# Kernel optimization log

Measured on AMD Instinct MI355X. Metric: run time of the kernel, lower is better.

Reference implementation:

```python
import jax, jax.numpy as jnp
import numpy as np

L, B, C = 512, 64, 512  # seq_len, batch, tags_size


def setup_inputs() -> dict:
    key = jax.random.key(0)
    k1, k2, k3, k4, k5, k6 = jax.random.split(key, 6)
    std = (1.0 / C) ** 0.5
    emit = jax.random.normal(k1, (L, B, C), dtype=jnp.float32)
    trans = jax.random.normal(k2, (C, C), dtype=jnp.float32) * std
    trans_from_start = jax.random.normal(k3, (C,), dtype=jnp.float32) * std
    trans_to_end = jax.random.normal(k4, (C,), dtype=jnp.float32) * std
    target = jax.random.randint(k5, (L, B), 0, C)
    # left-aligned length mask so mask.sum(0)-1 indexes the last valid step
    lens = jax.random.randint(k6, (B,), L // 2, L + 1)
    mask = jnp.arange(L)[:, None] < lens[None, :]
    return {"emit": emit, "target": target, "mask": mask, "trans": trans,
            "trans_from_start": trans_from_start, "trans_to_end": trans_to_end}


def _log_z(emit, mask, trans, trans_from_start, trans_to_end):
    log_alpha0 = emit[0] + trans_from_start  # (B, C)

    def step(log_alpha, xs):
        e_i, m_i = xs  # (B, C), (B,)
        # scores[b, j] = logsumexp_i( log_alpha[b, i] + trans[i, j] + e_i[b, j] )
        s = jax.nn.logsumexp(log_alpha[:, :, None] + trans[None, :, :] + e_i[:, None, :], axis=1)
        log_alpha = jnp.where(m_i[:, None], s, log_alpha)
        return log_alpha, None

    log_alpha, _ = jax.lax.scan(step, log_alpha0, (emit[1:], mask[1:]))
    return jax.nn.logsumexp(log_alpha + trans_to_end, axis=1).sum()


def _score(emit, target, mask, trans, trans_from_start, trans_to_end):
    l, b, c = emit.shape
    tr = trans[target[:-1], target[1:]]  # (L-1, B)
    scores = jnp.concatenate([jnp.zeros((1, b), emit.dtype), tr], axis=0)
    scores = scores + jnp.take_along_axis(emit, target[:, :, None], axis=2)[..., 0]
    score = jnp.where(mask, scores, jnp.zeros((), emit.dtype)).sum()
    ends = mask.sum(axis=0) - 1  # (B,) index of last valid step
    last_tags = target[ends, jnp.arange(b)]
    score = score + trans_from_start[target[0]].sum() + trans_to_end[last_tags].sum()
    return score


def reference(emit, target, mask, trans, trans_from_start, trans_to_end):
    b = emit.shape[1]
    log_z = _log_z(emit, mask, trans, trans_from_start, trans_to_end)
    score = _score(emit, target, mask, trans, trans_from_start, trans_to_end)
    return (log_z - score) / b
```

## Files before the change

kernel.cpp:

```cpp
#include <hip/hip_runtime.h>
#include <hip/hip_bf16.h>
#include <stdint.h>

#define LL 512
#define BB 64
#define CC 512
#define TM 255

typedef float float4v __attribute__((ext_vector_type(4)));
typedef int   int4v   __attribute__((ext_vector_type(4)));
typedef unsigned int uint4v __attribute__((ext_vector_type(4)));
typedef int   int8v  __attribute__((ext_vector_type(8)));

#define WS_ET     262144
#define WS_SCORE  524288
#define WS_SVA    524292
#define WS_SVB    524548
#define WS_ALPHA  528384
#define WS_BETA   659456


__device__ __forceinline__ bool mask_at(const void* maskp, bool is_byte, int t, int b) {
    if (is_byte) return ((const unsigned char*)maskp)[t * BB + b] != 0;
    return ((const int*)maskp)[t * BB + b] != 0;
}

__device__ __forceinline__ float rowmax16_dpp(float x) {
    int t;
    t = __builtin_amdgcn_update_dpp(0, __float_as_int(x), 0x128, 0xF, 0xF, true);
    x = fmaxf(x, __int_as_float(t));
    t = __builtin_amdgcn_update_dpp(0, __float_as_int(x), 0x124, 0xF, 0xF, true);
    x = fmaxf(x, __int_as_float(t));
    t = __builtin_amdgcn_update_dpp(0, __float_as_int(x), 0x122, 0xF, 0xF, true);
    x = fmaxf(x, __int_as_float(t));
    t = __builtin_amdgcn_update_dpp(0, __float_as_int(x), 0x121, 0xF, 0xF, true);
    x = fmaxf(x, __int_as_float(t));
    return x;
}

__device__ __forceinline__ void step_barrier() {
    asm volatile("s_waitcnt lgkmcnt(0)" ::: "memory");
    __builtin_amdgcn_sched_barrier(0);
    __builtin_amdgcn_s_barrier();
    asm volatile("" ::: "memory");
}

__global__ void prep_kernel(const float* __restrict__ trans, unsigned char* __restrict__ ws) {
    int g = blockIdx.x * blockDim.x + threadIdx.x;
    if (g == 0) *(float*)(ws + WS_SCORE) = 0.0f;
    if (g >= 512 * 128) return;
    int n  = g & 511;
    int pd = g >> 9;
    int wv = pd >> 4, rw = pd & 15;
    float f[4], ft[4];
#pragma unroll
    for (int nt = 0; nt < 4; ++nt) {
        int k = 64 * wv + 16 * nt + rw;
        f[nt]  = __expf(trans[(size_t)k * CC + n]);
        ft[nt] = __expf(trans[(size_t)n * CC + k]);
    }
    int r = 0;
    r = __builtin_amdgcn_cvt_pk_fp8_f32(f[0], f[1], r, false);
    r = __builtin_amdgcn_cvt_pk_fp8_f32(f[2], f[3], r, true);
    ((int*)ws)[n * 128 + pd] = r;
    int r2 = 0;
    r2 = __builtin_amdgcn_cvt_pk_fp8_f32(ft[0], ft[1], r2, false);
    r2 = __builtin_amdgcn_cvt_pk_fp8_f32(ft[2], ft[3], r2, true);
    ((int*)(ws + WS_ET))[n * 128 + pd] = r2;
}

__launch_bounds__(512, 2)
__global__ void crf_scan_kernel(const float* __restrict__ emit,
                                const int* __restrict__ target,
                                const void* __restrict__ maskp,
                                const float* __restrict__ trans,
                                const float* __restrict__ tfs,
                                const float* __restrict__ t2e,
                                unsigned char* __restrict__ ws) {
    const int tid = threadIdx.x;
    const bool is_byte = ((const unsigned char*)maskp)[1] != 0;

    if (blockIdx.x >= 8) {
        int sb = blockIdx.x - 8;
        float val = 0.0f;
        for (int e = sb * 512 + tid; e < LL * BB; e += 32 * 512) {
            int t = e >> 6, b = e & 63;
            if (mask_at(maskp, is_byte, t, b)) {
                int tg  = target[t * BB + b];
                float v = emit[(size_t)(t * BB + b) * CC + tg];
                if (t > 0) v += trans[(size_t)target[(t - 1) * BB + b] * CC + tg];
                val += v;
            }
        }
        if (sb == 0 && tid < BB) {
            int b = tid;
            val += tfs[target[b]];
            int lo = 0, hi = LL;
            while (lo < hi) {
                int mid = (lo + hi) >> 1;
                if (mask_at(maskp, is_byte, mid, b)) lo = mid + 1; else hi = mid;
            }
            val += t2e[target[(lo - 1) * BB + b]];
        }
        for (int off = 32; off > 0; off >>= 1) val += __shfl_down(val, off);
        if ((tid & 63) == 0) atomicAdd((float*)(ws + WS_SCORE), val);
        return;
    }

    const bool is_fwd = blockIdx.x < 4;
    const int B0 = (is_fwd ? blockIdx.x : blockIdx.x - 4) * 16;

    __shared__ __align__(16) unsigned char p8[2][16 * 528];
    __shared__ __align__(16) float mslotW[2][8][16];
    __shared__ float m0S[16];
    __shared__ float red[16][32];
    __shared__ int   lenS[16];
    __shared__ float mInitS;

    const int wv   = tid >> 6;
    const int lane = tid & 63;
    const int q    = lane >> 4;
    const int r15  = lane & 15;

    const unsigned char* ews = ws + (is_fwd ? 0 : WS_ET);
    int8v ef[4][4];
#pragma unroll
    for (int nt = 0; nt < 4; ++nt) {
        int n = (wv * 4 + nt) * 16 + r15;
#pragma unroll
        for (int kk4 = 0; kk4 < 4; ++kk4) {
            const unsigned char* src = ews + n * 512 + kk4 * 128 + q * 32;
            int4v lo = *(const int4v*)(src);
            int4v hi = *(const int4v*)(src + 16);
            ef[nt][kk4] = __builtin_shufflevector(lo, hi, 0, 1, 2, 3, 4, 5, 6, 7);
        }
    }

    const int c5 = tid >> 5;
    const int s5 = tid & 31;

    if (is_fwd) {
        {
            float lmax = -3.0e38f;
#pragma unroll
            for (int i = 0; i < 4; ++i) {
                int j4 = s5 + 32 * i;
                float4v em = *(const float4v*)(emit + (size_t)(B0 + c5) * CC + 4 * j4);
                float4v tf = *(const float4v*)(tfs + 4 * j4);
                float4v a = em + tf;
                lmax = fmaxf(lmax, fmaxf(fmaxf(a.x, a.y), fmaxf(a.z, a.w)));
            }
            red[c5][s5] = lmax;
        }
        __syncthreads();
        if (tid < 16) {
            float m0 = red[tid][0];
            for (int s = 1; s < 32; ++s) m0 = fmaxf(m0, red[tid][s]);
            m0S[tid] = m0;
        }
        if (tid < 128) ((float*)&mslotW[0][0][0])[tid] = 1.0f;
        __syncthreads();
        {
            float m0 = m0S[c5];
#pragma unroll
            for (int i = 0; i < 4; ++i) {
                int pd = s5 + 32 * i;
                int wvv = pd >> 4, rw = pd & 15;
                float f[4];
#pragma unroll
                for (int nt = 0; nt < 4; ++nt) {
                    int k = 64 * wvv + 16 * nt + rw;
                    f[nt] = __expf(emit[(size_t)(B0 + c5) * CC + k] + tfs[k] - m0);
                }
                int r = 0;
                r = __builtin_amdgcn_cvt_pk_fp8_f32(f[0], f[1], r, false);
                r = __builtin_amdgcn_cvt_pk_fp8_f32(f[2], f[3], r, true);
                *(int*)(&p8[0][0] + c5 * 528 + pd * 4) = r;
            }
        }
        __syncthreads();
    } else {
        {
            float m = t2e[tid];
            for (int off = 32; off > 0; off >>= 1) m = fmaxf(m, __shfl_xor(m, off));
            if (lane == 0) ((float*)red)[wv] = m;
        }
        __syncthreads();
        if (tid == 0) {
            float m = ((float*)red)[0];
            for (int i = 1; i < 8; ++i) m = fmaxf(m, ((float*)red)[i]);
            mInitS = __expf(m);
        }
        __syncthreads();
        {
#pragma unroll
            for (int i = 0; i < 4; ++i) {
                int pd = s5 + 32 * i;
                int wvv = pd >> 4, rw = pd & 15;
                float f[4];
#pragma unroll
                for (int nt = 0; nt < 4; ++nt)
                    f[nt] = __expf(t2e[64 * wvv + 16 * nt + rw]);
                int r = 0;
                r = __builtin_amdgcn_cvt_pk_fp8_f32(f[0], f[1], r, false);
                r = __builtin_amdgcn_cvt_pk_fp8_f32(f[2], f[3], r, true);
                *(int*)(&p8[0][0] + c5 * 528 + pd * 4) = r;
                *(int*)(&p8[1][0] + c5 * 528 + pd * 4) = r;
            }
            int part = 0;
            for (int k = 0; k < 16; ++k)
                part += mask_at(maskp, is_byte, s5 * 16 + k, B0 + c5) ? 1 : 0;
            red[c5][s5] = (float)part;
        }
        __syncthreads();
        if (tid < 16) {
            int s = 0;
            for (int i = 0; i < 32; ++i) s += (int)red[tid][i];
            lenS[tid] = s;
        }
        __syncthreads();
    }

    int4v gsum = {0, 0, 0, 0};
    const float4v z4 = {0.f, 0.f, 0.f, 0.f};

    if (is_fwd) {
        const float* eb0 = emit + (size_t)(BB + B0 + q * 4) * CC + (wv * 64 + r15);
        const float* eb1 = eb0 + 2 * CC;
        float4v ex4[4];
#pragma unroll
        for (int nt = 0; nt < 4; ++nt) {
            ex4[nt][0] = __expf(eb0[0 * CC + nt * 16]);
            ex4[nt][1] = __expf(eb0[1 * CC + nt * 16]);
            ex4[nt][2] = __expf(eb1[0 * CC + nt * 16]);
            ex4[nt][3] = __expf(eb1[1 * CC + nt * 16]);
        }

#pragma unroll 2
        for (int t = 1; t <= TM; ++t) {
            const int wp = t & 1;
            const int rp = wp ^ 1;
            eb0 += BB * CC;
            eb1 += BB * CC;

            const unsigned char* pr = &p8[rp][0] + r15 * 528 + q * 32;
            int8v af[4];
#pragma unroll
            for (int kk4 = 0; kk4 < 4; ++kk4) {
                int4v lo = *(const int4v*)(pr + kk4 * 128);
                int4v hi = *(const int4v*)(pr + kk4 * 128 + 16);
                af[kk4] = __builtin_shufflevector(lo, hi, 0, 1, 2, 3, 4, 5, 6, 7);
            }

            const char* mb = (const char*)&mslotW[(t - 1) & 1][0][q * 4];
            uint4v mm = *(const uint4v*)(mb);
#pragma unroll
            for (int i = 1; i < 8; ++i)
                mm = __builtin_elementwise_max(mm, *(const uint4v*)(mb + i * 64));

            float4v emn4[4];
#pragma unroll
            for (int nt = 0; nt < 4; ++nt) {
                emn4[nt][0] = eb0[0 * CC + nt * 16];
                emn4[nt][1] = eb0[1 * CC + nt * 16];
                emn4[nt][2] = eb1[0 * CC + nt * 16];
                emn4[nt][3] = eb1[1 * CC + nt * 16];
            }

            int4v e4 = {(int)(mm[0] >> 23), (int)(mm[1] >> 23), (int)(mm[2] >> 23), (int)(mm[3] >> 23)};
            int4v s2b = (248 - e4) << 23;
            float4v s24;
            s24[0] = __int_as_float(s2b[0]); s24[1] = __int_as_float(s2b[1]);
            s24[2] = __int_as_float(s2b[2]); s24[3] = __int_as_float(s2b[3]);

            float4v acc[4];
#pragma unroll
            for (int nt = 0; nt < 4; ++nt) acc[nt] = z4;

#pragma unroll
            for (int kk4 = 0; kk4 < 4; ++kk4)
#pragma unroll
                for (int nt = 0; nt < 2; ++nt)
                    acc[nt] = __builtin_amdgcn_mfma_scale_f32_16x16x128_f8f6f4(
                        af[kk4], ef[nt][kk4], acc[nt],
                        0, 0, 0, 0x7F7F7F7F, 0, 0x7F7F7F7F);

            float4v exn4[4];
#pragma unroll
            for (int nt = 0; nt < 4; ++nt) {
                exn4[nt][0] = __expf(emn4[nt][0]);
                exn4[nt][1] = __expf(emn4[nt][1]);
                exn4[nt][2] = __expf(emn4[nt][2]);
                exn4[nt][3] = __expf(emn4[nt][3]);
            }

#pragma unroll
            for (int kk4 = 0; kk4 < 4; ++kk4)
#pragma unroll
                for (int nt = 2; nt < 4; ++nt)
                    acc[nt] = __builtin_amdgcn_mfma_scale_f32_16x16x128_f8f6f4(
                        af[kk4], ef[nt][kk4], acc[nt],
                        0, 0, 0, 0x7F7F7F7F, 0, 0x7F7F7F7F);

            float4v p4[4];
#pragma unroll
            for (int nt = 0; nt < 4; ++nt) {
                float4v exr = ex4[nt] * s24;
                p4[nt] = acc[nt] * exr;
            }

            if (t == TM) {
                float* wA = (float*)(ws + WS_ALPHA) + (size_t)(B0 + q * 4) * CC + (wv * 64 + r15);
#pragma unroll
                for (int nt = 0; nt < 4; ++nt)
#pragma unroll
                    for (int rr = 0; rr < 4; ++rr)
                        wA[(size_t)rr * CC + nt * 16] = p4[nt][rr];
            }

            {
                float4v rm4 = __builtin_elementwise_max(
                    __builtin_elementwise_max(p4[0], p4[1]),
                    __builtin_elementwise_max(p4[2], p4[3]));
                float4v rw;
#pragma unroll
                for (int rr = 0; rr < 4; ++rr) rw[rr] = rowmax16_dpp(rm4[rr]);
                if (r15 == 0)
                    *(float4v*)&mslotW[t & 1][wv][q * 4] = rw;
            }

            {
                unsigned char* wrow = &p8[wp][0] + (wv * 16 + r15) * 4;
#pragma unroll
                for (int rr = 0; rr < 4; ++rr) {
                    float p0 = fminf(p4[0][rr], 448.0f);
                    float p1 = fminf(p4[1][rr], 448.0f);
                    float p2 = fminf(p4[2][rr], 448.0f);
                    float p3 = fminf(p4[3][rr], 448.0f);
                    int r = 0;
                    r = __builtin_amdgcn_cvt_pk_fp8_f32(p0, p1, r, false);
                    r = __builtin_amdgcn_cvt_pk_fp8_f32(p2, p3, r, true);
                    *(int*)(wrow + (q * 4 + rr) * 528) = r;
                }
            }

            if (wv == 0 && r15 == 0) gsum += (e4 - 121);

#pragma unroll
            for (int nt = 0; nt < 4; ++nt) ex4[nt] = exn4[nt];
            step_barrier();
        }
        if (wv == 0 && r15 == 0) {
#pragma unroll
            for (int rr = 0; rr < 4; ++rr)
                ((float*)(ws + WS_SVA))[B0 + q * 4 + rr] =
                    m0S[q * 4 + rr] + 0.6931471805599453f * (float)gsum[rr];
        }
    } else {
        int lenR[4];
#pragma unroll
        for (int rr = 0; rr < 4; ++rr) lenR[rr] = lenS[q * 4 + rr];
        const int eInit = __float_as_int(mInitS) >> 23;

        const float* eb0 = emit + ((size_t)(LL - 1) * BB + B0 + q * 4) * CC + (wv * 64 + r15);
        const float* eb1 = eb0 + 2 * CC;
        float4v ex4[4];
#pragma unroll
        for (int nt = 0; nt < 4; ++nt) {
            ex4[nt][0] = __expf(eb0[0 * CC + nt * 16]);
            ex4[nt][1] = __expf(eb0[1 * CC + nt * 16]);
            ex4[nt][2] = __expf(eb1[0 * CC + nt * 16]);
            ex4[nt][3] = __expf(eb1[1 * CC + nt * 16]);
        }

#pragma unroll 2
        for (int it = 0; it < 256; ++it) {
            const int t  = 510 - it;
            const int wp = it & 1;
            const int rp = wp ^ 1;
            eb0 -= BB * CC;
            eb1 -= BB * CC;

            const unsigned char* pr = &p8[rp][0] + r15 * 528 + q * 32;
            int8v af[4];
#pragma unroll
            for (int kk4 = 0; kk4 < 4; ++kk4) {
                int4v lo = *(const int4v*)(pr + kk4 * 128);
                int4v hi = *(const int4v*)(pr + kk4 * 128 + 16);
                af[kk4] = __builtin_shufflevector(lo, hi, 0, 1, 2, 3, 4, 5, 6, 7);
            }

            const char* mb = (const char*)&mslotW[(it - 1) & 1][0][q * 4];
            uint4v mm = *(const uint4v*)(mb);
#pragma unroll
            for (int i = 1; i < 8; ++i)
                mm = __builtin_elementwise_max(mm, *(const uint4v*)(mb + i * 64));

            float4v emn4[4];
#pragma unroll
            for (int nt = 0; nt < 4; ++nt) {
                emn4[nt][0] = eb0[0 * CC + nt * 16];
                emn4[nt][1] = eb0[1 * CC + nt * 16];
                emn4[nt][2] = eb1[0 * CC + nt * 16];
                emn4[nt][3] = eb1[1 * CC + nt * 16];
            }

            int4v e4 = {(int)(mm[0] >> 23), (int)(mm[1] >> 23), (int)(mm[2] >> 23), (int)(mm[3] >> 23)};
            int4v eU;
            float4v s2U;
#pragma unroll
            for (int rr = 0; rr < 4; ++rr) {
                bool ui = (t >= lenR[rr] - 2);
                int e = ui ? eInit : e4[rr];
                eU[rr] = e;
                s2U[rr] = __int_as_float((248 - e) << 23);
            }

            float4v acc[4];
#pragma unroll
            for (int nt = 0; nt < 4; ++nt) acc[nt] = z4;

#pragma unroll
            for (int kk4 = 0; kk4 < 4; ++kk4)
#pragma unroll
                for (int nt = 0; nt < 2; ++nt)
                    acc[nt] = __builtin_amdgcn_mfma_scale_f32_16x16x128_f8f6f4(
                        af[kk4], ef[nt][kk4], acc[nt],
                        0, 0, 0, 0x7F7F7F7F, 0, 0x7F7F7F7F);

            float4v exn4[4];
#pragma unroll
            for (int nt = 0; nt < 4; ++nt) {
                exn4[nt][0] = __expf(emn4[nt][0]);
                exn4[nt][1] = __expf(emn4[nt][1]);
                exn4[nt][2] = __expf(emn4[nt][2]);
                exn4[nt][3] = __expf(emn4[nt][3]);
            }

#pragma unroll
            for (int kk4 = 0; kk4 < 4; ++kk4)
#pragma unroll
                for (int nt = 2; nt < 4; ++nt)
                    acc[nt] = __builtin_amdgcn_mfma_scale_f32_16x16x128_f8f6f4(
                        af[kk4], ef[nt][kk4], acc[nt],
                        0, 0, 0, 0x7F7F7F7F, 0, 0x7F7F7F7F);

            float4v p4[4];
#pragma unroll
            for (int nt = 0; nt < 4; ++nt) {
                float4v exr = ex4[nt] * s2U;
                p4[nt] = acc[nt] * exr;
            }

            if (t == TM) {
                float* wB = (float*)(ws + WS_BETA) + (size_t)(B0 + q * 4) * CC + (wv * 64 + r15);
#pragma unroll
                for (int nt = 0; nt < 4; ++nt) {
                    float e2 = __expf(t2e[wv * 64 + nt * 16 + r15]);
#pragma unroll
                    for (int rr = 0; rr < 4; ++rr)
                        wB[(size_t)rr * CC + nt * 16] = (t <= lenR[rr] - 2) ? p4[nt][rr] : e2;
                }
            }

            {
                float4v rm4 = __builtin_elementwise_max(
                    __builtin_elementwise_max(p4[0], p4[1]),
                    __builtin_elementwise_max(p4[2], p4[3]));
                float4v rw;
#pragma unroll
                for (int rr = 0; rr < 4; ++rr) rw[rr] = rowmax16_dpp(rm4[rr]);
                if (r15 == 0)
                    *(float4v*)&mslotW[it & 1][wv][q * 4] = rw;
            }

            {
                unsigned char* wrow = &p8[wp][0] + (wv * 16 + r15) * 4;
#pragma unroll
                for (int rr = 0; rr < 4; ++rr) {
                    float p0 = fminf(p4[0][rr], 448.0f);
                    float p1 = fminf(p4[1][rr], 448.0f);
                    float p2 = fminf(p4[2][rr], 448.0f);
                    float p3 = fminf(p4[3][rr], 448.0f);
                    int r = 0;
                    r = __builtin_amdgcn_cvt_pk_fp8_f32(p0, p1, r, false);
                    r = __builtin_amdgcn_cvt_pk_fp8_f32(p2, p3, r, true);
                    if (t <= lenR[rr] - 2)
                        *(int*)(wrow + (q * 4 + rr) * 528) = r;
                }
            }

            if (wv == 0 && r15 == 0) {
#pragma unroll
                for (int rr = 0; rr < 4; ++rr)
                    if (t <= lenR[rr] - 2) gsum[rr] += (eU[rr] - 121);
            }

#pragma unroll
            for (int nt = 0; nt < 4; ++nt) ex4[nt] = exn4[nt];
            step_barrier();
        }
        if (wv == 0 && r15 == 0) {
#pragma unroll
            for (int rr = 0; rr < 4; ++rr)
                ((float*)(ws + WS_SVB))[B0 + q * 4 + rr] =
                    0.6931471805599453f * (float)gsum[rr];
        }
    }
}

__global__ void combine_kernel(const unsigned char* __restrict__ ws, float* __restrict__ out) {
    __shared__ float acc8[8];
    const int tid = threadIdx.x;
    const int c  = tid >> 3;
    const int s8 = tid & 7;
    const float* A = (const float*)(ws + WS_ALPHA) + (size_t)c * CC;
    const float* B = (const float*)(ws + WS_BETA)  + (size_t)c * CC;
    float d = 0.0f;
    for (int i = s8; i < CC; i += 8) d += A[i] * B[i];
    d += __shfl_xor(d, 1);
    d += __shfl_xor(d, 2);
    d += __shfl_xor(d, 4);
    float v = 0.0f;
    if (s8 == 0)
        v = ((const float*)(ws + WS_SVA))[c] + ((const float*)(ws + WS_SVB))[c] + __logf(d);
    for (int off = 32; off > 0; off >>= 1) v += __shfl_down(v, off);
    if ((tid & 63) == 0) acc8[tid >> 6] = v;
    __syncthreads();
    if (tid == 0) {
        float s = 0.0f;
        for (int i = 0; i < 8; ++i) s += acc8[i];
        out[0] = (s - *(const float*)(ws + WS_SCORE)) * (1.0f / 64.0f);
    }
}

extern "C" void kernel_launch(void* const* d_in, const int* in_sizes, int n_in,
                              void* d_out, int out_size, void* d_ws, size_t ws_size,
                              hipStream_t stream) {
    const float* emit   = (const float*)d_in[0];
    const int*   target = (const int*)d_in[1];
    const void*  maskp  = d_in[2];
    const float* trans  = (const float*)d_in[3];
    const float* tfs    = (const float*)d_in[4];
    const float* t2e    = (const float*)d_in[5];
    unsigned char* ws   = (unsigned char*)d_ws;
    float* out          = (float*)d_out;

    prep_kernel<<<256, 256, 0, stream>>>(trans, ws);
    crf_scan_kernel<<<40, 512, 0, stream>>>(emit, target, maskp, trans, tfs, t2e, ws);
    combine_kernel<<<1, 512, 0, stream>>>(ws, out);
}
```

Before: 492.9 us.

## Fuse combine into scan kernel and split MFMA halves to overlap pack/exp

```diff
diff --git a/kernel.cpp b/kernel.cpp
--- a/kernel.cpp
+++ b/kernel.cpp
@@ -16,6 +16,7 @@
 #define WS_SCORE  524288
 #define WS_SVA    524292
 #define WS_SVB    524548
+#define WS_CTR    524804
 #define WS_ALPHA  528384
 #define WS_BETA   659456
 
@@ -47,7 +48,7 @@
 
 __global__ void prep_kernel(const float* __restrict__ trans, unsigned char* __restrict__ ws) {
     int g = blockIdx.x * blockDim.x + threadIdx.x;
-    if (g == 0) *(float*)(ws + WS_SCORE) = 0.0f;
+    if (g == 0) { *(float*)(ws + WS_SCORE) = 0.0f; *(int*)(ws + WS_CTR) = 0; }
     if (g >= 512 * 128) return;
     int n  = g & 511;
     int pd = g >> 9;
@@ -76,11 +77,13 @@
                                 const float* __restrict__ trans,
                                 const float* __restrict__ tfs,
                                 const float* __restrict__ t2e,
-                                unsigned char* __restrict__ ws) {
+                                unsigned char* __restrict__ ws,
+                                float* __restrict__ out) {
     const int tid = threadIdx.x;
     const bool is_byte = ((const unsigned char*)maskp)[1] != 0;
 
     if (blockIdx.x >= 8) {
+        __shared__ float acc8[8];
         int sb = blockIdx.x - 8;
         float val = 0.0f;
         for (int e = sb * 512 + tid; e < LL * BB; e += 32 * 512) {
@@ -104,6 +107,36 @@
         }
         for (int off = 32; off > 0; off >>= 1) val += __shfl_down(val, off);
         if ((tid & 63) == 0) atomicAdd((float*)(ws + WS_SCORE), val);
+        __syncthreads();
+        if (tid == 0) { __threadfence(); atomicAdd((int*)(ws + WS_CTR), 1); }
+
+        if (blockIdx.x == 39) {
+            if (tid == 0) {
+                while (atomicAdd((int*)(ws + WS_CTR), 0) < 40) __builtin_amdgcn_s_sleep(2);
+                __threadfence();
+            }
+            __syncthreads();
+            const int c  = tid >> 3;
+            const int s8 = tid & 7;
+            const float* A = (const float*)(ws + WS_ALPHA) + (size_t)c * CC;
+            const float* B = (const float*)(ws + WS_BETA)  + (size_t)c * CC;
+            float d = 0.0f;
+            for (int i = s8; i < CC; i += 8) d += A[i] * B[i];
+            d += __shfl_xor(d, 1);
+            d += __shfl_xor(d, 2);
+            d += __shfl_xor(d, 4);
+            float v = 0.0f;
+            if (s8 == 0)
+                v = ((const float*)(ws + WS_SVA))[c] + ((const float*)(ws + WS_SVB))[c] + __logf(d);
+            for (int off = 32; off > 0; off >>= 1) v += __shfl_down(v, off);
+            if ((tid & 63) == 0) acc8[tid >> 6] = v;
+            __syncthreads();
+            if (tid == 0) {
+                float s = 0.0f;
+                for (int i = 0; i < 8; ++i) s += acc8[i];
+                out[0] = (s - *(const float*)(ws + WS_SCORE)) * (1.0f / 64.0f);
+            }
+        }
         return;
     }
 
@@ -251,7 +284,6 @@
                 int4v hi = *(const int4v*)(pr + kk4 * 128 + 16);
                 af[kk4] = __builtin_shufflevector(lo, hi, 0, 1, 2, 3, 4, 5, 6, 7);
             }
-
             const char* mb = (const char*)&mslotW[(t - 1) & 1][0][q * 4];
             uint4v mm = *(const uint4v*)(mb);
 #pragma unroll
@@ -267,61 +299,65 @@
                 emn4[nt][3] = eb1[1 * CC + nt * 16];
             }
 
+            float4v acc0 = z4, acc1 = z4, acc2 = z4, acc3 = z4;
+#pragma unroll
+            for (int kk4 = 0; kk4 < 4; ++kk4) {
+                acc0 = __builtin_amdgcn_mfma_scale_f32_16x16x128_f8f6f4(
+                    af[kk4], ef[0][kk4], acc0, 0, 0, 0, 0x7F7F7F7F, 0, 0x7F7F7F7F);
+                acc1 = __builtin_amdgcn_mfma_scale_f32_16x16x128_f8f6f4(
+                    af[kk4], ef[1][kk4], acc1, 0, 0, 0, 0x7F7F7F7F, 0, 0x7F7F7F7F);
+            }
+
             int4v e4 = {(int)(mm[0] >> 23), (int)(mm[1] >> 23), (int)(mm[2] >> 23), (int)(mm[3] >> 23)};
             int4v s2b = (248 - e4) << 23;
             float4v s24;
             s24[0] = __int_as_float(s2b[0]); s24[1] = __int_as_float(s2b[1]);
             s24[2] = __int_as_float(s2b[2]); s24[3] = __int_as_float(s2b[3]);
 
-            float4v acc[4];
-#pragma unroll
-            for (int nt = 0; nt < 4; ++nt) acc[nt] = z4;
-
-#pragma unroll
-            for (int kk4 = 0; kk4 < 4; ++kk4)
-#pragma unroll
-                for (int nt = 0; nt < 2; ++nt)
-                    acc[nt] = __builtin_amdgcn_mfma_scale_f32_16x16x128_f8f6f4(
-                        af[kk4], ef[nt][kk4], acc[nt],
-                        0, 0, 0, 0x7F7F7F7F, 0, 0x7F7F7F7F);
-
-            float4v exn4[4];
-#pragma unroll
-            for (int nt = 0; nt < 4; ++nt) {
-                exn4[nt][0] = __expf(emn4[nt][0]);
-                exn4[nt][1] = __expf(emn4[nt][1]);
-                exn4[nt][2] = __expf(emn4[nt][2]);
-                exn4[nt][3] = __expf(emn4[nt][3]);
-            }
-
-#pragma unroll
-            for (int kk4 = 0; kk4 < 4; ++kk4)
-#pragma unroll
-                for (int nt = 2; nt < 4; ++nt)
-                    acc[nt] = __builtin_amdgcn_mfma_scale_f32_16x16x128_f8f6f4(
-                        af[kk4], ef[nt][kk4], acc[nt],
-                        0, 0, 0, 0x7F7F7F7F, 0, 0x7F7F7F7F);
-
-            float4v p4[4];
-#pragma unroll
-            for (int nt = 0; nt < 4; ++nt) {
-                float4v exr = ex4[nt] * s24;
-                p4[nt] = acc[nt] * exr;
-            }
-
-            if (t == TM) {
-                float* wA = (float*)(ws + WS_ALPHA) + (size_t)(B0 + q * 4) * CC + (wv * 64 + r15);
-#pragma unroll
-                for (int nt = 0; nt < 4; ++nt)
-#pragma unroll
-                    for (int rr = 0; rr < 4; ++rr)
-                        wA[(size_t)rr * CC + nt * 16] = p4[nt][rr];
-            }
-
+            float4v p0 = acc0 * (ex4[0] * s24);
+            float4v p1 = acc1 * (ex4[1] * s24);
+            float4v rmA = __builtin_elementwise_max(p0, p1);
             {
-                float4v rm4 = __builtin_elementwise_max(
-                    __builtin_elementwise_max(p4[0], p4[1]),
-                    __builtin_elementwise_max(p4[2], p4[3]));
+                unsigned char* wrow = &p8[wp][0] + (wv * 16 + r15) * 4;
+#pragma unroll
+                for (int rr = 0; rr < 4; ++rr) {
+                    int r = __builtin_amdgcn_cvt_pk_fp8_f32(
+                        fminf(p0[rr], 448.0f), fminf(p1[rr], 448.0f), 0, false);
+                    *(short*)(wrow + (q * 4 + rr) * 528) = (short)r;
+                }
+            }
+            ex4[0][0] = __expf(emn4[0][0]); ex4[0][1] = __expf(emn4[0][1]);
+            ex4[0][2] = __expf(emn4[0][2]); ex4[0][3] = __expf(emn4[0][3]);
+            ex4[1][0] = __expf(emn4[1][0]); ex4[1][1] = __expf(emn4[1][1]);
+            ex4[1][2] = __expf(emn4[1][2]); ex4[1][3] = __expf(emn4[1][3]);
+
+#pragma unroll
+            for (int kk4 = 0; kk4 < 4; ++kk4) {
+                acc2 = __builtin_amdgcn_mfma_scale_f32_16x16x128_f8f6f4(
+                    af[kk4], ef[2][kk4], acc2, 0, 0, 0, 0x7F7F7F7F, 0, 0x7F7F7F7F);
+                acc3 = __builtin_amdgcn_mfma_scale_f32_16x16x128_f8f6f4(
+                    af[kk4], ef[3][kk4], acc3, 0, 0, 0, 0x7F7F7F7F, 0, 0x7F7F7F7F);
+            }
+
+            float4v p2 = acc2 * (ex4[2] * s24);
+            float4v p3 = acc3 * (ex4[3] * s24);
+            float4v rmB = __builtin_elementwise_max(p2, p3);
+            {
+                unsigned char* wrow = &p8[wp][0] + (wv * 16 + r15) * 4;
+#pragma unroll
+                for (int rr = 0; rr < 4; ++rr) {
+                    int r = __builtin_amdgcn_cvt_pk_fp8_f32(
+                        fminf(p2[rr], 448.0f), fminf(p3[rr], 448.0f), 0, false);
+                    *(short*)(wrow + (q * 4 + rr) * 528 + 2) = (short)r;
+                }
+            }
+            ex4[2][0] = __expf(emn4[2][0]); ex4[2][1] = __expf(emn4[2][1]);
+            ex4[2][2] = __expf(emn4[2][2]); ex4[2][3] = __expf(emn4[2][3]);
+            ex4[3][0] = __expf(emn4[3][0]); ex4[3][1] = __expf(emn4[3][1]);
+            ex4[3][2] = __expf(emn4[3][2]); ex4[3][3] = __expf(emn4[3][3]);
+
+            {
+                float4v rm4 = __builtin_elementwise_max(rmA, rmB);
                 float4v rw;
 #pragma unroll
                 for (int rr = 0; rr < 4; ++rr) rw[rr] = rowmax16_dpp(rm4[rr]);
@@ -329,25 +365,18 @@
                     *(float4v*)&mslotW[t & 1][wv][q * 4] = rw;
             }
 
-            {
-                unsigned char* wrow = &p8[wp][0] + (wv * 16 + r15) * 4;
+            gsum += (e4 - 121);
+
+            if (t == TM) {
+                float* wA = (float*)(ws + WS_ALPHA) + (size_t)(B0 + q * 4) * CC + (wv * 64 + r15);
 #pragma unroll
                 for (int rr = 0; rr < 4; ++rr) {
-                    float p0 = fminf(p4[0][rr], 448.0f);
-                    float p1 = fminf(p4[1][rr], 448.0f);
-                    float p2 = fminf(p4[2][rr], 448.0f);
-                    float p3 = fminf(p4[3][rr], 448.0f);
-                    int r = 0;
-                    r = __builtin_amdgcn_cvt_pk_fp8_f32(p0, p1, r, false);
-                    r = __builtin_amdgcn_cvt_pk_fp8_f32(p2, p3, r, true);
-                    *(int*)(wrow + (q * 4 + rr) * 528) = r;
-                }
-            }
-
-            if (wv == 0 && r15 == 0) gsum += (e4 - 121);
-
-#pragma unroll
-            for (int nt = 0; nt < 4; ++nt) ex4[nt] = exn4[nt];
+                    wA[(size_t)rr * CC +  0] = p0[rr];
+                    wA[(size_t)rr * CC + 16] = p1[rr];
+                    wA[(size_t)rr * CC + 32] = p2[rr];
+                    wA[(size_t)rr * CC + 48] = p3[rr];
+                }
+            }
             step_barrier();
         }
         if (wv == 0 && r15 == 0) {
@@ -361,6 +390,14 @@
 #pragma unroll
         for (int rr = 0; rr < 4; ++rr) lenR[rr] = lenS[q * 4 + rr];
         const int eInit = __float_as_int(mInitS) >> 23;
+
+        int rInit = 0;
+        rInit = __builtin_amdgcn_cvt_pk_fp8_f32(__expf(t2e[64 * wv + r15]),
+                                                __expf(t2e[64 * wv + 16 + r15]), rInit, false);
+        rInit = __builtin_amdgcn_cvt_pk_fp8_f32(__expf(t2e[64 * wv + 32 + r15]),
+                                                __expf(t2e[64 * wv + 48 + r15]), rInit, true);
+        const short rInitLo = (short)(rInit & 0xffff);
+        const short rInitHi = (short)(((unsigned)rInit) >> 16);
 
         const float* eb0 = emit + ((size_t)(LL - 1) * BB + B0 + q * 4) * CC + (wv * 64 + r15);
         const float* eb1 = eb0 + 2 * CC;
@@ -389,7 +426,6 @@
                 int4v hi = *(const int4v*)(pr + kk4 * 128 + 16);
                 af[kk4] = __builtin_shufflevector(lo, hi, 0, 1, 2, 3, 4, 5, 6, 7);
             }
-
             const char* mb = (const char*)&mslotW[(it - 1) & 1][0][q * 4];
             uint4v mm = *(const uint4v*)(mb);
 #pragma unroll
@@ -405,68 +441,72 @@
                 emn4[nt][3] = eb1[1 * CC + nt * 16];
             }
 
+            float4v acc0 = z4, acc1 = z4, acc2 = z4, acc3 = z4;
+#pragma unroll
+            for (int kk4 = 0; kk4 < 4; ++kk4) {
+                acc0 = __builtin_amdgcn_mfma_scale_f32_16x16x128_f8f6f4(
+                    af[kk4], ef[0][kk4], acc0, 0, 0, 0, 0x7F7F7F7F, 0, 0x7F7F7F7F);
+                acc1 = __builtin_amdgcn_mfma_scale_f32_16x16x128_f8f6f4(
+                    af[kk4], ef[1][kk4], acc1, 0, 0, 0, 0x7F7F7F7F, 0, 0x7F7F7F7F);
+            }
+
             int4v e4 = {(int)(mm[0] >> 23), (int)(mm[1] >> 23), (int)(mm[2] >> 23), (int)(mm[3] >> 23)};
             int4v eU;
             float4v s2U;
+            bool lv[4];
 #pragma unroll
             for (int rr = 0; rr < 4; ++rr) {
                 bool ui = (t >= lenR[rr] - 2);
+                lv[rr] = (t <= lenR[rr] - 2);
                 int e = ui ? eInit : e4[rr];
                 eU[rr] = e;
                 s2U[rr] = __int_as_float((248 - e) << 23);
             }
 
-            float4v acc[4];
-#pragma unroll
-            for (int nt = 0; nt < 4; ++nt) acc[nt] = z4;
-
-#pragma unroll
-            for (int kk4 = 0; kk4 < 4; ++kk4)
-#pragma unroll
-                for (int nt = 0; nt < 2; ++nt)
-                    acc[nt] = __builtin_amdgcn_mfma_scale_f32_16x16x128_f8f6f4(
-                        af[kk4], ef[nt][kk4], acc[nt],
-                        0, 0, 0, 0x7F7F7F7F, 0, 0x7F7F7F7F);
-
-            float4v exn4[4];
-#pragma unroll
-            for (int nt = 0; nt < 4; ++nt) {
-                exn4[nt][0] = __expf(emn4[nt][0]);
-                exn4[nt][1] = __expf(emn4[nt][1]);
-                exn4[nt][2] = __expf(emn4[nt][2]);
-                exn4[nt][3] = __expf(emn4[nt][3]);
-            }
-
-#pragma unroll
-            for (int kk4 = 0; kk4 < 4; ++kk4)
-#pragma unroll
-                for (int nt = 2; nt < 4; ++nt)
-                    acc[nt] = __builtin_amdgcn_mfma_scale_f32_16x16x128_f8f6f4(
-                        af[kk4], ef[nt][kk4], acc[nt],
-                        0, 0, 0, 0x7F7F7F7F, 0, 0x7F7F7F7F);
-
-            float4v p4[4];
-#pragma unroll
-            for (int nt = 0; nt < 4; ++nt) {
-                float4v exr = ex4[nt] * s2U;
-                p4[nt] = acc[nt] * exr;
-            }
-
-            if (t == TM) {
-                float* wB = (float*)(ws + WS_BETA) + (size_t)(B0 + q * 4) * CC + (wv * 64 + r15);
-#pragma unroll
-                for (int nt = 0; nt < 4; ++nt) {
-                    float e2 = __expf(t2e[wv * 64 + nt * 16 + r15]);
-#pragma unroll
-                    for (int rr = 0; rr < 4; ++rr)
-                        wB[(size_t)rr * CC + nt * 16] = (t <= lenR[rr] - 2) ? p4[nt][rr] : e2;
-                }
-            }
-
+            float4v p0 = acc0 * (ex4[0] * s2U);
+            float4v p1 = acc1 * (ex4[1] * s2U);
+            float4v rmA = __builtin_elementwise_max(p0, p1);
             {
-                float4v rm4 = __builtin_elementwise_max(
-                    __builtin_elementwise_max(p4[0], p4[1]),
-                    __builtin_elementwise_max(p4[2], p4[3]));
+                unsigned char* wrow = &p8[wp][0] + (wv * 16 + r15) * 4;
+#pragma unroll
+                for (int rr = 0; rr < 4; ++rr) {
+                    int r = __builtin_amdgcn_cvt_pk_fp8_f32(
+                        fminf(p0[rr], 448.0f), fminf(p1[rr], 448.0f), 0, false);
+                    *(short*)(wrow + (q * 4 + rr) * 528) = lv[rr] ? (short)r : rInitLo;
+                }
+            }
+            ex4[0][0] = __expf(emn4[0][0]); ex4[0][1] = __expf(emn4[0][1]);
+            ex4[0][2] = __expf(emn4[0][2]); ex4[0][3] = __expf(emn4[0][3]);
+            ex4[1][0] = __expf(emn4[1][0]); ex4[1][1] = __expf(emn4[1][1]);
+            ex4[1][2] = __expf(emn4[1][2]); ex4[1][3] = __expf(emn4[1][3]);
+
+#pragma unroll
+            for (int kk4 = 0; kk4 < 4; ++kk4) {
+                acc2 = __builtin_amdgcn_mfma_scale_f32_16x16x128_f8f6f4(
+                    af[kk4], ef[2][kk4], acc2, 0, 0, 0, 0x7F7F7F7F, 0, 0x7F7F7F7F);
+                acc3 = __builtin_amdgcn_mfma_scale_f32_16x16x128_f8f6f4(
+                    af[kk4], ef[3][kk4], acc3, 0, 0, 0, 0x7F7F7F7F, 0, 0x7F7F7F7F);
+            }
+
+            float4v p2 = acc2 * (ex4[2] * s2U);
+            float4v p3 = acc3 * (ex4[3] * s2U);
+            float4v rmB = __builtin_elementwise_max(p2, p3);
+            {
+                unsigned char* wrow = &p8[wp][0] + (wv * 16 + r15) * 4;
+#pragma unroll
+                for (int rr = 0; rr < 4; ++rr) {
+                    int r = __builtin_amdgcn_cvt_pk_fp8_f32(
+                        fminf(p2[rr], 448.0f), fminf(p3[rr], 448.0f), 0, false);
+                    *(short*)(wrow + (q * 4 + rr) * 528 + 2) = lv[rr] ? (short)r : rInitHi;
+                }
+            }
+            ex4[2][0] = __expf(emn4[2][0]); ex4[2][1] = __expf(emn4[2][1]);
+            ex4[2][2] = __expf(emn4[2][2]); ex4[2][3] = __expf(emn4[2][3]);
+            ex4[3][0] = __expf(emn4[3][0]); ex4[3][1] = __expf(emn4[3][1]);
+            ex4[3][2] = __expf(emn4[3][2]); ex4[3][3] = __expf(emn4[3][3]);
+
+            {
+                float4v rm4 = __builtin_elementwise_max(rmA, rmB);
                 float4v rw;
 #pragma unroll
                 for (int rr = 0; rr < 4; ++rr) rw[rr] = rowmax16_dpp(rm4[rr]);
@@ -474,30 +514,21 @@
                     *(float4v*)&mslotW[it & 1][wv][q * 4] = rw;
             }
 
-            {
-                unsigned char* wrow = &p8[wp][0] + (wv * 16 + r15) * 4;
-#pragma unroll
-                for (int rr = 0; rr < 4; ++rr) {
-                    float p0 = fminf(p4[0][rr], 448.0f);
-                    float p1 = fminf(p4[1][rr], 448.0f);
-                    float p2 = fminf(p4[2][rr], 448.0f);
-                    float p3 = fminf(p4[3][rr], 448.0f);
-                    int r = 0;
-                    r = __builtin_amdgcn_cvt_pk_fp8_f32(p0, p1, r, false);
-                    r = __builtin_amdgcn_cvt_pk_fp8_f32(p2, p3, r, true);
-                    if (t <= lenR[rr] - 2)
-                        *(int*)(wrow + (q * 4 + rr) * 528) = r;
-                }
-            }
-
-            if (wv == 0 && r15 == 0) {
-#pragma unroll
-                for (int rr = 0; rr < 4; ++rr)
-                    if (t <= lenR[rr] - 2) gsum[rr] += (eU[rr] - 121);
-            }
-
-#pragma unroll
-            for (int nt = 0; nt < 4; ++nt) ex4[nt] = exn4[nt];
+#pragma unroll
+            for (int rr = 0; rr < 4; ++rr)
+                gsum[rr] += lv[rr] ? (eU[rr] - 121) : 0;
+
+            if (t == TM) {
+                float* wB = (float*)(ws + WS_BETA) + (size_t)(B0 + q * 4) * CC + (wv * 64 + r15);
+#pragma unroll
+                for (int nt = 0; nt < 4; ++nt) {
+                    float e2 = __expf(t2e[wv * 64 + nt * 16 + r15]);
+                    const float4v& psel = (nt == 0) ? p0 : (nt == 1) ? p1 : (nt == 2) ? p2 : p3;
+#pragma unroll
+                    for (int rr = 0; rr < 4; ++rr)
+                        wB[(size_t)rr * CC + nt * 16] = lv[rr] ? psel[rr] : e2;
+                }
+            }
             step_barrier();
         }
         if (wv == 0 && r15 == 0) {
@@ -507,31 +538,9 @@
                     0.6931471805599453f * (float)gsum[rr];
         }
     }
-}
-
-__global__ void combine_kernel(const unsigned char* __restrict__ ws, float* __restrict__ out) {
-    __shared__ float acc8[8];
-    const int tid = threadIdx.x;
-    const int c  = tid >> 3;
-    const int s8 = tid & 7;
-    const float* A = (const float*)(ws + WS_ALPHA) + (size_t)c * CC;
-    const float* B = (const float*)(ws + WS_BETA)  + (size_t)c * CC;
-    float d = 0.0f;
-    for (int i = s8; i < CC; i += 8) d += A[i] * B[i];
-    d += __shfl_xor(d, 1);
-    d += __shfl_xor(d, 2);
-    d += __shfl_xor(d, 4);
-    float v = 0.0f;
-    if (s8 == 0)
-        v = ((const float*)(ws + WS_SVA))[c] + ((const float*)(ws + WS_SVB))[c] + __logf(d);
-    for (int off = 32; off > 0; off >>= 1) v += __shfl_down(v, off);
-    if ((tid & 63) == 0) acc8[tid >> 6] = v;
+
     __syncthreads();
-    if (tid == 0) {
-        float s = 0.0f;
-        for (int i = 0; i < 8; ++i) s += acc8[i];
-        out[0] = (s - *(const float*)(ws + WS_SCORE)) * (1.0f / 64.0f);
-    }
+    if (tid == 0) { __threadfence(); atomicAdd((int*)(ws + WS_CTR), 1); }
 }
 
 extern "C" void kernel_launch(void* const* d_in, const int* in_sizes, int n_in,
@@ -547,6 +556,5 @@
     float* out          = (float*)d_out;
 
     prep_kernel<<<256, 256, 0, stream>>>(trans, ws);
-    crf_scan_kernel<<<40, 512, 0, stream>>>(emit, target, maskp, trans, tfs, t2e, ws);
-    combine_kernel<<<1, 512, 0, stream>>>(ws, out);
+    crf_scan_kernel<<<40, 512, 0, stream>>>(emit, target, maskp, trans, tfs, t2e, ws, out);
 }
```

Result: slower. 567.3 us (+15.1%).

## Fuse prep and combine kernels into scan kernel with atomic-counter grid sync

Applied to the files above, without the earlier changes.

```diff
diff --git a/kernel.cpp b/kernel.cpp
--- a/kernel.cpp
+++ b/kernel.cpp
@@ -14,8 +14,10 @@
 
 #define WS_ET     262144
 #define WS_SCORE  524288
-#define WS_SVA    524292
-#define WS_SVB    524548
+#define WS_CTR    524292
+#define WS_CTR2   524296
+#define WS_SVA    524352
+#define WS_SVB    524608
 #define WS_ALPHA  528384
 #define WS_BETA   659456
 
@@ -45,30 +47,6 @@
     asm volatile("" ::: "memory");
 }
 
-__global__ void prep_kernel(const float* __restrict__ trans, unsigned char* __restrict__ ws) {
-    int g = blockIdx.x * blockDim.x + threadIdx.x;
-    if (g == 0) *(float*)(ws + WS_SCORE) = 0.0f;
-    if (g >= 512 * 128) return;
-    int n  = g & 511;
-    int pd = g >> 9;
-    int wv = pd >> 4, rw = pd & 15;
-    float f[4], ft[4];
-#pragma unroll
-    for (int nt = 0; nt < 4; ++nt) {
-        int k = 64 * wv + 16 * nt + rw;
-        f[nt]  = __expf(trans[(size_t)k * CC + n]);
-        ft[nt] = __expf(trans[(size_t)n * CC + k]);
-    }
-    int r = 0;
-    r = __builtin_amdgcn_cvt_pk_fp8_f32(f[0], f[1], r, false);
-    r = __builtin_amdgcn_cvt_pk_fp8_f32(f[2], f[3], r, true);
-    ((int*)ws)[n * 128 + pd] = r;
-    int r2 = 0;
-    r2 = __builtin_amdgcn_cvt_pk_fp8_f32(ft[0], ft[1], r2, false);
-    r2 = __builtin_amdgcn_cvt_pk_fp8_f32(ft[2], ft[3], r2, true);
-    ((int*)(ws + WS_ET))[n * 128 + pd] = r2;
-}
-
 __launch_bounds__(512, 2)
 __global__ void crf_scan_kernel(const float* __restrict__ emit,
                                 const int* __restrict__ target,
@@ -76,12 +54,41 @@
                                 const float* __restrict__ trans,
                                 const float* __restrict__ tfs,
                                 const float* __restrict__ t2e,
-                                unsigned char* __restrict__ ws) {
+                                unsigned char* __restrict__ ws,
+                                float* __restrict__ out) {
     const int tid = threadIdx.x;
     const bool is_byte = ((const unsigned char*)maskp)[1] != 0;
 
     if (blockIdx.x >= 8) {
+        __shared__ float acc8[8];
         int sb = blockIdx.x - 8;
+
+#pragma unroll
+        for (int i = 0; i < 4; ++i) {
+            int g  = sb * 512 + tid + i * 16384;
+            int n  = g & 511;
+            int pd = g >> 9;
+            int wvp = pd >> 4, rw = pd & 15;
+            float f[4], ft[4];
+#pragma unroll
+            for (int nt = 0; nt < 4; ++nt) {
+                int k = 64 * wvp + 16 * nt + rw;
+                f[nt]  = __expf(trans[(size_t)k * CC + n]);
+                ft[nt] = __expf(trans[(size_t)n * CC + k]);
+            }
+            int r = 0;
+            r = __builtin_amdgcn_cvt_pk_fp8_f32(f[0], f[1], r, false);
+            r = __builtin_amdgcn_cvt_pk_fp8_f32(f[2], f[3], r, true);
+            ((int*)ws)[n * 128 + pd] = r;
+            int r2 = 0;
+            r2 = __builtin_amdgcn_cvt_pk_fp8_f32(ft[0], ft[1], r2, false);
+            r2 = __builtin_amdgcn_cvt_pk_fp8_f32(ft[2], ft[3], r2, true);
+            ((int*)(ws + WS_ET))[n * 128 + pd] = r2;
+        }
+        __threadfence();
+        __syncthreads();
+        if (tid == 0) atomicAdd((int*)(ws + WS_CTR2), 1);
+
         float val = 0.0f;
         for (int e = sb * 512 + tid; e < LL * BB; e += 32 * 512) {
             int t = e >> 6, b = e & 63;
@@ -104,6 +111,37 @@
         }
         for (int off = 32; off > 0; off >>= 1) val += __shfl_down(val, off);
         if ((tid & 63) == 0) atomicAdd((float*)(ws + WS_SCORE), val);
+        __threadfence();
+        __syncthreads();
+        if (tid == 0) atomicAdd((int*)(ws + WS_CTR), 1);
+
+        if (blockIdx.x == 39) {
+            if (tid == 0) {
+                while (atomicAdd((int*)(ws + WS_CTR), 0) < 40) __builtin_amdgcn_s_sleep(2);
+            }
+            __syncthreads();
+            __threadfence();
+            const int c  = tid >> 3;
+            const int s8 = tid & 7;
+            const float* A = (const float*)(ws + WS_ALPHA) + (size_t)c * CC;
+            const float* B = (const float*)(ws + WS_BETA)  + (size_t)c * CC;
+            float d = 0.0f;
+            for (int i = s8; i < CC; i += 8) d += A[i] * B[i];
+            d += __shfl_xor(d, 1);
+            d += __shfl_xor(d, 2);
+            d += __shfl_xor(d, 4);
+            float v = 0.0f;
+            if (s8 == 0)
+                v = ((const float*)(ws + WS_SVA))[c] + ((const float*)(ws + WS_SVB))[c] + __logf(d);
+            for (int off = 32; off > 0; off >>= 1) v += __shfl_down(v, off);
+            if ((tid & 63) == 0) acc8[tid >> 6] = v;
+            __syncthreads();
+            if (tid == 0) {
+                float s = 0.0f;
+                for (int i = 0; i < 8; ++i) s += acc8[i];
+                out[0] = (s - *(const float*)(ws + WS_SCORE)) * (1.0f / 64.0f);
+            }
+        }
         return;
     }
 
@@ -121,21 +159,6 @@
     const int lane = tid & 63;
     const int q    = lane >> 4;
     const int r15  = lane & 15;
-
-    const unsigned char* ews = ws + (is_fwd ? 0 : WS_ET);
-    int8v ef[4][4];
-#pragma unroll
-    for (int nt = 0; nt < 4; ++nt) {
-        int n = (wv * 4 + nt) * 16 + r15;
-#pragma unroll
-        for (int kk4 = 0; kk4 < 4; ++kk4) {
-            const unsigned char* src = ews + n * 512 + kk4 * 128 + q * 32;
-            int4v lo = *(const int4v*)(src);
-            int4v hi = *(const int4v*)(src + 16);
-            ef[nt][kk4] = __builtin_shufflevector(lo, hi, 0, 1, 2, 3, 4, 5, 6, 7);
-        }
-    }
-
     const int c5 = tid >> 5;
     const int s5 = tid & 31;
 
@@ -219,6 +242,26 @@
             lenS[tid] = s;
         }
         __syncthreads();
+    }
+
+    if (tid == 0) {
+        while (atomicAdd((int*)(ws + WS_CTR2), 0) < 32) __builtin_amdgcn_s_sleep(2);
+    }
+    __syncthreads();
+    __threadfence();
+
+    const unsigned char* ews = ws + (is_fwd ? 0 : WS_ET);
+    int8v ef[4][4];
+#pragma unroll
+    for (int nt = 0; nt < 4; ++nt) {
+        int n = (wv * 4 + nt) * 16 + r15;
+#pragma unroll
+        for (int kk4 = 0; kk4 < 4; ++kk4) {
+            const unsigned char* src = ews + n * 512 + kk4 * 128 + q * 32;
+            int4v lo = *(const int4v*)(src);
+            int4v hi = *(const int4v*)(src + 16);
+            ef[nt][kk4] = __builtin_shufflevector(lo, hi, 0, 1, 2, 3, 4, 5, 6, 7);
+        }
     }
 
     int4v gsum = {0, 0, 0, 0};
@@ -507,31 +550,10 @@
                     0.6931471805599453f * (float)gsum[rr];
         }
     }
-}
-
-__global__ void combine_kernel(const unsigned char* __restrict__ ws, float* __restrict__ out) {
-    __shared__ float acc8[8];
-    const int tid = threadIdx.x;
-    const int c  = tid >> 3;
-    const int s8 = tid & 7;
-    const float* A = (const float*)(ws + WS_ALPHA) + (size_t)c * CC;
-    const float* B = (const float*)(ws + WS_BETA)  + (size_t)c * CC;
-    float d = 0.0f;
-    for (int i = s8; i < CC; i += 8) d += A[i] * B[i];
-    d += __shfl_xor(d, 1);
-    d += __shfl_xor(d, 2);
-    d += __shfl_xor(d, 4);
-    float v = 0.0f;
-    if (s8 == 0)
-        v = ((const float*)(ws + WS_SVA))[c] + ((const float*)(ws + WS_SVB))[c] + __logf(d);
-    for (int off = 32; off > 0; off >>= 1) v += __shfl_down(v, off);
-    if ((tid & 63) == 0) acc8[tid >> 6] = v;
+
+    __threadfence();
     __syncthreads();
-    if (tid == 0) {
-        float s = 0.0f;
-        for (int i = 0; i < 8; ++i) s += acc8[i];
-        out[0] = (s - *(const float*)(ws + WS_SCORE)) * (1.0f / 64.0f);
-    }
+    if (tid == 0) atomicAdd((int*)(ws + WS_CTR), 1);
 }
 
 extern "C" void kernel_launch(void* const* d_in, const int* in_sizes, int n_in,
@@ -546,7 +568,6 @@
     unsigned char* ws   = (unsigned char*)d_ws;
     float* out          = (float*)d_out;
 
-    prep_kernel<<<256, 256, 0, stream>>>(trans, ws);
-    crf_scan_kernel<<<40, 512, 0, stream>>>(emit, target, maskp, trans, tfs, t2e, ws);
-    combine_kernel<<<1, 512, 0, stream>>>(ws, out);
+    hipMemsetAsync(ws + WS_SCORE, 0, 12, stream);
+    crf_scan_kernel<<<40, 512, 0, stream>>>(emit, target, maskp, trans, tfs, t2e, ws, out);
 }
```

New measurement: 519.8 us. +5.5%, slower.
